# Performance work log

Hardware: AMD Instinct MI355X
Metric: run time of the kernel (lower is better)

## Reference

```python
import jax, jax.numpy as jnp
import numpy as np

B, T, J, E = 64, 512, 64, 128
D = 2 * E  # bidaf feature dim


def _lstm_dir(x, Wih, Whh, bih, bhh, reverse):
    # x: (B, S, I); PyTorch gate order i, f, g, o
    H = Whh.shape[1]
    b = bih + bhh
    xs = jnp.swapaxes(x, 0, 1)  # (S, B, I)
    if reverse:
        xs = xs[::-1]
    pre = jnp.einsum('sbi,gi->sbg', xs, Wih) + b  # precompute input projections
    h0 = jnp.zeros((x.shape[0], H), x.dtype)

    def step(carry, pt):
        h, c = carry
        gates = pt + h @ Whh.T
        i, f, g, o = jnp.split(gates, 4, axis=-1)
        c = jax.nn.sigmoid(f) * c + jax.nn.sigmoid(i) * jnp.tanh(g)
        h = jax.nn.sigmoid(o) * jnp.tanh(c)
        return (h, c), h

    _, hs = jax.lax.scan(step, (h0, h0), pre)
    if reverse:
        hs = hs[::-1]
    return jnp.swapaxes(hs, 0, 1)  # (B, S, H)


def _bilstm(x, pf, pb):
    hf = _lstm_dir(x, pf[0], pf[1], pf[2], pf[3], False)
    hb = _lstm_dir(x, pb[0], pb[1], pb[2], pb[3], True)
    return jnp.concatenate([hf, hb], axis=-1)


def setup_inputs() -> dict:
    key = jax.random.key(0)
    ks = iter(jax.random.split(key, 40))

    def rn(shape, scale=0.05):
        return jax.random.normal(next(ks), shape, jnp.float32) * scale

    inp = {
        'c': jax.random.normal(next(ks), (B, T, D), jnp.float32),
        'q': jax.random.normal(next(ks), (B, J, D), jnp.float32),
        # trilinear attention weights (Linear(2E,1) each)
        'wc': rn((D,)), 'bc': rn((1,)),
        'wq': rn((D,)), 'bq': rn((1,)),
        'wcq': rn((D,)), 'bcq': rn((1,)),
        # modeling BiLSTM: input 8E -> hidden E, bidirectional
        'l1f_Wih': rn((4 * E, 8 * E)), 'l1f_Whh': rn((4 * E, E)), 'l1f_bih': rn((4 * E,)), 'l1f_bhh': rn((4 * E,)),
        'l1b_Wih': rn((4 * E, 8 * E)), 'l1b_Whh': rn((4 * E, E)), 'l1b_bih': rn((4 * E,)), 'l1b_bhh': rn((4 * E,)),
        # output BiLSTM: input 2E -> hidden E, bidirectional
        'l2f_Wih': rn((4 * E, 2 * E)), 'l2f_Whh': rn((4 * E, E)), 'l2f_bih': rn((4 * E,)), 'l2f_bhh': rn((4 * E,)),
        'l2b_Wih': rn((4 * E, 2 * E)), 'l2b_Whh': rn((4 * E, E)), 'l2b_bih': rn((4 * E,)), 'l2b_bhh': rn((4 * E,)),
        # span predictors Linear(10E, 1)
        'W0': rn((10 * E,)), 'b0': rn((1,)),
        'W1': rn((10 * E,)), 'b1': rn((1,)),
    }
    return inp


def reference(c, q, wc, bc, wq, bq, wcq, bcq,
              l1f_Wih, l1f_Whh, l1f_bih, l1f_bhh,
              l1b_Wih, l1b_Whh, l1b_bih, l1b_bhh,
              l2f_Wih, l2f_Whh, l2f_bih, l2f_bhh,
              l2b_Wih, l2b_Whh, l2b_bih, l2b_bhh,
              W0, b0, W1, b1):
    # fused trilinear similarity: replaces the python loop over q_len
    cq = jnp.einsum('btd,bjd,d->btj', c, q, wcq) + bcq[0]            # (B,T,J)
    s = (c @ wc + bc[0])[:, :, None] + (q @ wq + bq[0])[:, None, :] + cq
    a = jax.nn.softmax(s, axis=2)
    c2q = jnp.einsum('btj,bjd->btd', a, q)                            # context-to-query
    b_att = jax.nn.softmax(jnp.max(s, axis=2), axis=1)                # (B,T)
    q2c = jnp.einsum('bt,btd->bd', b_att, c)[:, None, :]              # (B,1,2E) broadcast over T
    g = jnp.concatenate([c, c2q, c * c2q, c * q2c * jnp.ones_like(c)], axis=-1)  # (B,T,8E)

    m = _bilstm(g, (l1f_Wih, l1f_Whh, l1f_bih, l1f_bhh), (l1b_Wih, l1b_Whh, l1b_bih, l1b_bhh))
    p1 = jax.nn.softmax(jnp.concatenate([g, m], axis=-1) @ W0 + b0[0], axis=1)
    m2 = _bilstm(m, (l2f_Wih, l2f_Whh, l2f_bih, l2f_bhh), (l2b_Wih, l2b_Whh, l2b_bih, l2b_bhh))
    p2 = jax.nn.softmax(jnp.concatenate([g, m2], axis=-1) @ W1 + b1[0], axis=1)
    return (p1, p2)
```

## Files before the change

kernel.cpp:

```cpp
#include <hip/hip_runtime.h>
#include <hip/hip_bf16.h>
#include <cstdint>
#include <cstddef>


typedef short short8v __attribute__((ext_vector_type(8)));
typedef float f32x4 __attribute__((ext_vector_type(4)));
typedef unsigned short ushort8v __attribute__((ext_vector_type(8)));
typedef unsigned short ushort4v __attribute__((ext_vector_type(4)));

static __device__ __forceinline__ float bf2f(unsigned short u) {
  return __uint_as_float(((unsigned int)u) << 16);
}
static __device__ __forceinline__ unsigned short f2bf(float f) {
  unsigned int u = __float_as_uint(f);
  return (unsigned short)((u + 0x7FFFu + ((u >> 16) & 1u)) >> 16);
}
static __device__ __forceinline__ float fsig(float x) {
  return 1.f / (1.f + __expf(-x));
}
static __device__ __forceinline__ float ftanh(float x) {
  return 1.f - 2.f / (__expf(2.f * x) + 1.f);
}

__global__ __launch_bounds__(256) void cvt_w_kernel(
    const float* __restrict__ w1f, const float* __restrict__ w1b,
    const float* __restrict__ w2f, const float* __restrict__ w2b,
    const float* __restrict__ b1fi, const float* __restrict__ b1fh,
    const float* __restrict__ b1bi, const float* __restrict__ b1bh,
    const float* __restrict__ b2fi, const float* __restrict__ b2fh,
    const float* __restrict__ b2bi, const float* __restrict__ b2bh,
    unsigned short* __restrict__ d1f, unsigned short* __restrict__ d1b,
    unsigned short* __restrict__ d2f, unsigned short* __restrict__ d2b,
    float* __restrict__ bs)
{
  const int bid = blockIdx.x, tid = threadIdx.x;
  if (bid < 1280) {
    int idx = (bid * 256 + tid) * 4;
    const float* src;
    unsigned short* dst;
    int off;
    if (idx < 524288)        { src = w1f; dst = d1f; off = idx; }
    else if (idx < 1048576)  { src = w1b; dst = d1b; off = idx - 524288; }
    else if (idx < 1179648)  { src = w2f; dst = d2f; off = idx - 1048576; }
    else                     { src = w2b; dst = d2b; off = idx - 1179648; }
    float4 f = *(const float4*)(src + off);
    ushort4v v;
    v[0] = f2bf(f.x); v[1] = f2bf(f.y); v[2] = f2bf(f.z); v[3] = f2bf(f.w);
    *(ushort4v*)(dst + off) = v;
  } else {
    int bidx = (bid - 1280) * 256 + tid;
    int which = bidx >> 9, col = bidx & 511;
    float v;
    if (which == 0)      v = b1fi[col] + b1fh[col];
    else if (which == 1) v = b1bi[col] + b1bh[col];
    else if (which == 2) v = b2fi[col] + b2fh[col];
    else                 v = b2bi[col] + b2bh[col];
    bs[bidx] = v;
  }
}

__global__ __launch_bounds__(256) void attn_kernel(
    const float* __restrict__ c, const float* __restrict__ q,
    const float* __restrict__ wc, const float* __restrict__ bc,
    const float* __restrict__ wq, const float* __restrict__ bq,
    const float* __restrict__ wcq, const float* __restrict__ bcq,
    const float* __restrict__ W0, const float* __restrict__ W1,
    __hip_bfloat16* __restrict__ g, float* __restrict__ smax,
    float* __restrict__ gz0, float* __restrict__ gz1)
{
  __shared__ float qr[64][256];
  __shared__ float qrt[256][64];
  __shared__ float qwqs[64];
  __shared__ float cwbuf[4][256];
  __shared__ float abuf[4][64];
  const int b = blockIdx.x;
  const int tid = threadIdx.x;
  for (int e = tid; e < 64 * 256; e += 256) {
    int j = e >> 8, d = e & 255;
    float v = q[((size_t)b * 64 + j) * 256 + d];
    qr[j][d] = v;
    qrt[d][j] = v;
  }
  __syncthreads();
  if (tid < 64) {
    float s = 0.f;
    for (int d = 0; d < 256; ++d) s += qrt[d][tid] * wq[d];
    qwqs[tid] = s + bq[0];
  }
  __syncthreads();
  const int wave = tid >> 6, lane = tid & 63;
  const float bcv = bc[0], bcqv = bcq[0];
  const int t0 = blockIdx.y * 128;
  for (int it = 0; it < 32; ++it) {
    const int trow = t0 + wave + it * 4;
    const float* crow = c + ((size_t)b * 512 + trow) * 256;
    float cv[4];
    float part = 0.f;
    #pragma unroll
    for (int r = 0; r < 4; ++r) {
      int d = lane + 64 * r;
      cv[r] = crow[d];
      cwbuf[wave][d] = cv[r] * wcq[d];
      part += cv[r] * wc[d];
    }
    #pragma unroll
    for (int off = 32; off; off >>= 1) part += __shfl_xor(part, off);
    float s = part + bcv + qwqs[lane] + bcqv;
    #pragma unroll 8
    for (int d = 0; d < 256; ++d) s += cwbuf[wave][d] * qrt[d][lane];
    float mx = s;
    #pragma unroll
    for (int off = 32; off; off >>= 1) mx = fmaxf(mx, __shfl_xor(mx, off));
    float e = expf(s - mx);
    float sum = e;
    #pragma unroll
    for (int off = 32; off; off >>= 1) sum += __shfl_xor(sum, off);
    abuf[wave][lane] = e / sum;
    const size_t grow = (size_t)b * 512 + trow;
    if (lane == 0) smax[grow] = mx;
    size_t row = grow * 1024;
    float az0 = 0.f, az1 = 0.f;
    #pragma unroll
    for (int r = 0; r < 4; ++r) {
      int d = lane + 64 * r;
      float acc = 0.f;
      #pragma unroll 8
      for (int j = 0; j < 64; ++j) acc += abuf[wave][j] * qr[j][d];
      float prod = cv[r] * acc;
      g[row + d]       = __float2bfloat16(cv[r]);
      g[row + 256 + d] = __float2bfloat16(acc);
      g[row + 512 + d] = __float2bfloat16(prod);
      az0 += cv[r] * W0[d] + acc * W0[256 + d] + prod * W0[512 + d];
      az1 += cv[r] * W1[d] + acc * W1[256 + d] + prod * W1[512 + d];
    }
    #pragma unroll
    for (int off = 32; off; off >>= 1) {
      az0 += __shfl_xor(az0, off);
      az1 += __shfl_xor(az1, off);
    }
    if (lane == 0) { gz0[grow] = az0; gz1[grow] = az1; }
  }
}

__global__ __launch_bounds__(256) void batt_kernel(
    const float* __restrict__ c, const float* __restrict__ smax,
    const float* __restrict__ W0, const float* __restrict__ W1,
    __hip_bfloat16* __restrict__ g,
    float* __restrict__ gz0, float* __restrict__ gz1)
{
  __shared__ float sm[512];
  __shared__ float red[4], red2[4];
  __shared__ float q2c_s[256];
  const int b = blockIdx.x, tid = threadIdx.x;
  float v0 = smax[(size_t)b * 512 + tid];
  float v1 = smax[(size_t)b * 512 + tid + 256];
  float m = fmaxf(v0, v1);
  #pragma unroll
  for (int off = 32; off; off >>= 1) m = fmaxf(m, __shfl_xor(m, off));
  if ((tid & 63) == 0) red[tid >> 6] = m;
  __syncthreads();
  float M = fmaxf(fmaxf(red[0], red[1]), fmaxf(red[2], red[3]));
  float e0 = expf(v0 - M), e1 = expf(v1 - M);
  float ssum = e0 + e1;
  #pragma unroll
  for (int off = 32; off; off >>= 1) ssum += __shfl_xor(ssum, off);
  if ((tid & 63) == 0) red2[tid >> 6] = ssum;
  __syncthreads();
  float S = red2[0] + red2[1] + red2[2] + red2[3];
  sm[tid] = e0 / S;
  sm[tid + 256] = e1 / S;
  __syncthreads();
  float acc = 0.f;
  #pragma unroll 8
  for (int t = 0; t < 512; ++t) acc += sm[t] * c[((size_t)b * 512 + t) * 256 + tid];
  q2c_s[tid] = acc;
  __syncthreads();
  const int wave = tid >> 6, lane = tid & 63;
  float qv[4], w0c[4], w1c[4];
  #pragma unroll
  for (int r = 0; r < 4; ++r) {
    int d = lane + 64 * r;
    qv[r]  = q2c_s[d];
    w0c[r] = W0[768 + d];
    w1c[r] = W1[768 + d];
  }
  for (int t = wave; t < 512; t += 4) {
    size_t row = (size_t)b * 512 + t;
    float s0 = 0.f, s1 = 0.f;
    #pragma unroll
    for (int r = 0; r < 4; ++r) {
      int d = lane + 64 * r;
      float v = c[row * 256 + d];
      float gv = v * qv[r];
      g[row * 1024 + 768 + d] = __float2bfloat16(gv);
      s0 += gv * w0c[r];
      s1 += gv * w1c[r];
    }
    #pragma unroll
    for (int off = 32; off; off >>= 1) {
      s0 += __shfl_xor(s0, off);
      s1 += __shfl_xor(s1, off);
    }
    if (lane == 0) { gz0[row] += s0; gz1[row] += s1; }
  }
}

__global__ __launch_bounds__(256) void gemm_mfma_kernel(
    const __hip_bfloat16* __restrict__ Xg,
    const unsigned short* __restrict__ Wf, const unsigned short* __restrict__ Wb,
    const float* __restrict__ bsf, const float* __restrict__ bsb,
    __hip_bfloat16* __restrict__ Yf, __hip_bfloat16* __restrict__ Yb, int K)
{
  __shared__ unsigned short Xs[128 * 72];
  __shared__ unsigned short Ws[128 * 72];
  const unsigned short* X = (const unsigned short*)Xg;
  const unsigned short* W = blockIdx.z ? Wb : Wf;
  const float* bs = blockIdx.z ? bsb : bsf;
  __hip_bfloat16* Y = blockIdx.z ? Yb : Yf;
  const int tid = threadIdx.x;
  const int m0 = blockIdx.x * 128, n0 = blockIdx.y * 128;
  const int lane = tid & 63, wave = tid >> 6;
  const int wr = wave >> 1, wc = wave & 1;
  const int frow = lane & 15, fk = (lane >> 4) * 8;

  f32x4 acc[4][4] = {};
  for (int kt = 0; kt < K; kt += 64) {
    #pragma unroll
    for (int i = 0; i < 4; ++i) {
      int cidx = tid + 256 * i;
      int row = cidx >> 3, kc = cidx & 7;
      *(ushort8v*)&Xs[row * 72 + kc * 8] =
          *(const ushort8v*)&X[(size_t)(m0 + row) * K + kt + kc * 8];
      *(ushort8v*)&Ws[row * 72 + kc * 8] =
          *(const ushort8v*)&W[(size_t)(n0 + row) * K + kt + kc * 8];
    }
    __syncthreads();
    #pragma unroll
    for (int kk = 0; kk < 64; kk += 32) {
      short8v a[4], bfr[4];
      #pragma unroll
      for (int i = 0; i < 4; ++i)
        a[i] = *(const short8v*)&Xs[(wr * 64 + i * 16 + frow) * 72 + kk + fk];
      #pragma unroll
      for (int j = 0; j < 4; ++j)
        bfr[j] = *(const short8v*)&Ws[(wc * 64 + j * 16 + frow) * 72 + kk + fk];
      #pragma unroll
      for (int i = 0; i < 4; ++i)
        #pragma unroll
        for (int j = 0; j < 4; ++j)
          acc[i][j] = __builtin_amdgcn_mfma_f32_16x16x32_bf16(a[i], bfr[j], acc[i][j], 0, 0, 0);
    }
    __syncthreads();
  }
  const int r0 = (lane >> 4) * 4;
  #pragma unroll
  for (int j = 0; j < 4; ++j) {
    int col = n0 + wc * 64 + j * 16 + (lane & 15);
    int colp = (col & 127) * 4 + (col >> 7);
    float bsum = bs[col];
    #pragma unroll
    for (int i = 0; i < 4; ++i) {
      int rowb = m0 + wr * 64 + i * 16 + r0;
      #pragma unroll
      for (int r = 0; r < 4; ++r)
        Y[(size_t)(rowb + r) * 512 + colp] = __float2bfloat16(acc[i][j][r] + bsum);
    }
  }
}

__global__ __launch_bounds__(512, 2) void lstm_kernel(
    const __hip_bfloat16* __restrict__ pre_f, const __hip_bfloat16* __restrict__ pre_b,
    const float* __restrict__ Whh_f, const float* __restrict__ Whh_b,
    __hip_bfloat16* __restrict__ out)
{
  const int b = blockIdx.x, dir = blockIdx.y;
  const unsigned short* __restrict__ pre =
      (const unsigned short*)(dir ? pre_b : pre_f);
  const float* __restrict__ Whh = dir ? Whh_b : Whh_f;
  const int off = dir ? 128 : 0;
  const int tid = threadIdx.x;
  const int wave = tid >> 6, lane = tid & 63;
  const int cl = lane & 15;
  const int kg = lane >> 4;
  const int cell = wave * 16 + cl;

#define LOAD_BF(Q, T, DST)                                            \
  {                                                                   \
    const float* wp = Whh + (size_t)(Q * 128 + cell) * 128 + T * 32 + kg * 8; \
    float4 f0 = *(const float4*)wp;                                   \
    float4 f1 = *(const float4*)(wp + 4);                             \
    DST[0] = (short)f2bf(f0.x); DST[1] = (short)f2bf(f0.y);           \
    DST[2] = (short)f2bf(f0.z); DST[3] = (short)f2bf(f0.w);           \
    DST[4] = (short)f2bf(f1.x); DST[5] = (short)f2bf(f1.y);           \
    DST[6] = (short)f2bf(f1.z); DST[7] = (short)f2bf(f1.w);           \
    asm volatile("" : "+v"(DST));                                     \
  }
  short8v bf00, bf01, bf02, bf03, bf10, bf11, bf12, bf13;
  short8v bf20, bf21, bf22, bf23, bf30, bf31, bf32, bf33;
  LOAD_BF(0, 0, bf00) LOAD_BF(0, 1, bf01) LOAD_BF(0, 2, bf02) LOAD_BF(0, 3, bf03)
  LOAD_BF(1, 0, bf10) LOAD_BF(1, 1, bf11) LOAD_BF(1, 2, bf12) LOAD_BF(1, 3, bf13)
  LOAD_BF(2, 0, bf20) LOAD_BF(2, 1, bf21) LOAD_BF(2, 2, bf22) LOAD_BF(2, 3, bf23)
  LOAD_BF(3, 0, bf30) LOAD_BF(3, 1, bf31) LOAD_BF(3, 2, bf32) LOAD_BF(3, 3, bf33)
#undef LOAD_BF

  __shared__ unsigned short hbuf[2][128];
  if (tid < 128) { hbuf[0][tid] = 0; hbuf[1][tid] = 0; }
  __syncthreads();

  const size_t base = (size_t)b * 512;
  const int tstep = dir ? -1 : 1;
  const int t0 = dir ? 511 : 0;
  const unsigned short* prow = pre + base * 512 + cell * 4;
  unsigned short* orow = (unsigned short*)out + base * 256 + off + cell;

  int cur = 0;
  float cst = 0.f;
  f32x4 acc0 = {0.f, 0.f, 0.f, 0.f};
  f32x4 acc1 = acc0, acc2 = acc0, acc3 = acc0;

#define LSTM_STEP(P, HOUT)                                                  \
  {                                                                         \
    const unsigned short* hb = hbuf[cur];                                   \
    short8v a0 = *(const short8v*)(hb +  0 + kg * 8);                       \
    short8v a1 = *(const short8v*)(hb + 32 + kg * 8);                       \
    short8v a2 = *(const short8v*)(hb + 64 + kg * 8);                       \
    short8v a3 = *(const short8v*)(hb + 96 + kg * 8);                       \
    acc0[0] = bf2f(P[0]); acc1[0] = bf2f(P[1]);                             \
    acc2[0] = bf2f(P[2]); acc3[0] = bf2f(P[3]);                             \
    acc0 = __builtin_amdgcn_mfma_f32_16x16x32_bf16(a0, bf00, acc0, 0, 0, 0);\
    acc1 = __builtin_amdgcn_mfma_f32_16x16x32_bf16(a0, bf10, acc1, 0, 0, 0);\
    acc2 = __builtin_amdgcn_mfma_f32_16x16x32_bf16(a0, bf20, acc2, 0, 0, 0);\
    acc3 = __builtin_amdgcn_mfma_f32_16x16x32_bf16(a0, bf30, acc3, 0, 0, 0);\
    acc0 = __builtin_amdgcn_mfma_f32_16x16x32_bf16(a1, bf01, acc0, 0, 0, 0);\
    acc1 = __builtin_amdgcn_mfma_f32_16x16x32_bf16(a1, bf11, acc1, 0, 0, 0);\
    acc2 = __builtin_amdgcn_mfma_f32_16x16x32_bf16(a1, bf21, acc2, 0, 0, 0);\
    acc3 = __builtin_amdgcn_mfma_f32_16x16x32_bf16(a1, bf31, acc3, 0, 0, 0);\
    acc0 = __builtin_amdgcn_mfma_f32_16x16x32_bf16(a2, bf02, acc0, 0, 0, 0);\
    acc1 = __builtin_amdgcn_mfma_f32_16x16x32_bf16(a2, bf12, acc1, 0, 0, 0);\
    acc2 = __builtin_amdgcn_mfma_f32_16x16x32_bf16(a2, bf22, acc2, 0, 0, 0);\
    acc3 = __builtin_amdgcn_mfma_f32_16x16x32_bf16(a2, bf32, acc3, 0, 0, 0);\
    acc0 = __builtin_amdgcn_mfma_f32_16x16x32_bf16(a3, bf03, acc0, 0, 0, 0);\
    acc1 = __builtin_amdgcn_mfma_f32_16x16x32_bf16(a3, bf13, acc1, 0, 0, 0);\
    acc2 = __builtin_amdgcn_mfma_f32_16x16x32_bf16(a3, bf23, acc2, 0, 0, 0);\
    acc3 = __builtin_amdgcn_mfma_f32_16x16x32_bf16(a3, bf33, acc3, 0, 0, 0);\
    float gi_ = fsig(acc0[0]);                                              \
    float gf_ = fsig(acc1[0]);                                              \
    float gg_ = ftanh(acc2[0]);                                             \
    float go_ = fsig(acc3[0]);                                              \
    cst = gf_ * cst + gi_ * gg_;                                            \
    float hv = go_ * ftanh(cst);                                            \
    HOUT = f2bf(hv);                                                        \
    if (lane < 16) hbuf[cur ^ 1][cell] = HOUT;                              \
    __syncthreads();                                                        \
    cur ^= 1;                                                               \
  }

  for (int chunk = 0; chunk < 64; ++chunk) {
    const int tb = t0 + chunk * 8 * tstep;
    ushort4v p0 = *(const ushort4v*)(prow + (size_t)(tb)             * 512);
    ushort4v p1 = *(const ushort4v*)(prow + (size_t)(tb + 1 * tstep) * 512);
    ushort4v p2 = *(const ushort4v*)(prow + (size_t)(tb + 2 * tstep) * 512);
    ushort4v p3 = *(const ushort4v*)(prow + (size_t)(tb + 3 * tstep) * 512);
    ushort4v p4 = *(const ushort4v*)(prow + (size_t)(tb + 4 * tstep) * 512);
    ushort4v p5 = *(const ushort4v*)(prow + (size_t)(tb + 5 * tstep) * 512);
    ushort4v p6 = *(const ushort4v*)(prow + (size_t)(tb + 6 * tstep) * 512);
    ushort4v p7 = *(const ushort4v*)(prow + (size_t)(tb + 7 * tstep) * 512);
    unsigned short h0, h1, h2, h3, h4, h5, h6, h7;
    LSTM_STEP(p0, h0)
    LSTM_STEP(p1, h1)
    LSTM_STEP(p2, h2)
    LSTM_STEP(p3, h3)
    LSTM_STEP(p4, h4)
    LSTM_STEP(p5, h5)
    LSTM_STEP(p6, h6)
    LSTM_STEP(p7, h7)
    if (lane < 16) {
      orow[(size_t)(tb)             * 256] = h0;
      orow[(size_t)(tb + 1 * tstep) * 256] = h1;
      orow[(size_t)(tb + 2 * tstep) * 256] = h2;
      orow[(size_t)(tb + 3 * tstep) * 256] = h3;
      orow[(size_t)(tb + 4 * tstep) * 256] = h4;
      orow[(size_t)(tb + 5 * tstep) * 256] = h5;
      orow[(size_t)(tb + 6 * tstep) * 256] = h6;
      orow[(size_t)(tb + 7 * tstep) * 256] = h7;
    }
  }
#undef LSTM_STEP
}

__global__ __launch_bounds__(256) void logits_kernel(
    const __hip_bfloat16* __restrict__ m, const float* __restrict__ W,
    const float* __restrict__ bias, const float* __restrict__ gz,
    float* __restrict__ z)
{
  const int row = blockIdx.x * 4 + (threadIdx.x >> 6);
  const int lane = threadIdx.x & 63;
  const unsigned short* mrow = (const unsigned short*)m + (size_t)row * 256;
  float acc = 0.f;
  #pragma unroll
  for (int i = 0; i < 4; ++i) acc += bf2f(mrow[lane + 64 * i]) * W[1024 + lane + 64 * i];
  #pragma unroll
  for (int off = 32; off; off >>= 1) acc += __shfl_xor(acc, off);
  if (lane == 0) z[row] = acc + gz[row] + bias[0];
}

__global__ __launch_bounds__(512) void softmax_t_kernel(
    const float* __restrict__ z, float* __restrict__ p)
{
  const int b = blockIdx.x, t = threadIdx.x;
  __shared__ float red[8], red2[8];
  float v = z[(size_t)b * 512 + t];
  float m = v;
  #pragma unroll
  for (int off = 32; off; off >>= 1) m = fmaxf(m, __shfl_xor(m, off));
  if ((t & 63) == 0) red[t >> 6] = m;
  __syncthreads();
  float M = red[0];
  #pragma unroll
  for (int i = 1; i < 8; ++i) M = fmaxf(M, red[i]);
  float e = expf(v - M);
  float s = e;
  #pragma unroll
  for (int off = 32; off; off >>= 1) s += __shfl_xor(s, off);
  if ((t & 63) == 0) red2[t >> 6] = s;
  __syncthreads();
  float S = red2[0];
  #pragma unroll
  for (int i = 1; i < 8; ++i) S += red2[i];
  p[(size_t)b * 512 + t] = e / S;
}

extern "C" void kernel_launch(void* const* d_in, const int* in_sizes, int n_in,
                              void* d_out, int out_size, void* d_ws, size_t ws_size,
                              hipStream_t stream)
{
  const float* c   = (const float*)d_in[0];
  const float* q   = (const float*)d_in[1];
  const float* wc  = (const float*)d_in[2];
  const float* bc  = (const float*)d_in[3];
  const float* wq  = (const float*)d_in[4];
  const float* bq  = (const float*)d_in[5];
  const float* wcq = (const float*)d_in[6];
  const float* bcq = (const float*)d_in[7];
  const float* l1f_Wih = (const float*)d_in[8];
  const float* l1f_Whh = (const float*)d_in[9];
  const float* l1f_bih = (const float*)d_in[10];
  const float* l1f_bhh = (const float*)d_in[11];
  const float* l1b_Wih = (const float*)d_in[12];
  const float* l1b_Whh = (const float*)d_in[13];
  const float* l1b_bih = (const float*)d_in[14];
  const float* l1b_bhh = (const float*)d_in[15];
  const float* l2f_Wih = (const float*)d_in[16];
  const float* l2f_Whh = (const float*)d_in[17];
  const float* l2f_bih = (const float*)d_in[18];
  const float* l2f_bhh = (const float*)d_in[19];
  const float* l2b_Wih = (const float*)d_in[20];
  const float* l2b_Whh = (const float*)d_in[21];
  const float* l2b_bih = (const float*)d_in[22];
  const float* l2b_bhh = (const float*)d_in[23];
  const float* W0 = (const float*)d_in[24];
  const float* b0 = (const float*)d_in[25];
  const float* W1 = (const float*)d_in[26];
  const float* b1 = (const float*)d_in[27];

  const size_t required = 137371648u;
  if (ws_size < required) return;

  char* wsb = (char*)d_ws;
  __hip_bfloat16* gbf = (__hip_bfloat16*)wsb;
  __hip_bfloat16* m   = (__hip_bfloat16*)wsb;
  __hip_bfloat16* m2  = (__hip_bfloat16*)(wsb + 33554432);
  __hip_bfloat16* pref = (__hip_bfloat16*)(wsb + 67108864);
  __hip_bfloat16* preb = (__hip_bfloat16*)(wsb + 100663296);
  float* gz0  = (float*)(wsb + 134217728);
  float* gz1  = gz0 + 32768;
  float* smax = gz1 + 32768;
  float* z    = smax + 32768;
  unsigned short* w1f = (unsigned short*)(wsb + 134742016);
  unsigned short* w1b = (unsigned short*)(wsb + 135790592);
  unsigned short* w2f = (unsigned short*)(wsb + 136839168);
  unsigned short* w2b = (unsigned short*)(wsb + 137101312);
  float* bs = (float*)(wsb + 137363456);
  float* p1 = (float*)d_out;
  float* p2 = p1 + 32768;

  cvt_w_kernel<<<1288, 256, 0, stream>>>(l1f_Wih, l1b_Wih, l2f_Wih, l2b_Wih,
                                         l1f_bih, l1f_bhh, l1b_bih, l1b_bhh,
                                         l2f_bih, l2f_bhh, l2b_bih, l2b_bhh,
                                         w1f, w1b, w2f, w2b, bs);
  attn_kernel<<<dim3(64, 4), 256, 0, stream>>>(c, q, wc, bc, wq, bq, wcq, bcq,
                                               W0, W1, gbf, smax, gz0, gz1);
  batt_kernel<<<64, 256, 0, stream>>>(c, smax, W0, W1, gbf, gz0, gz1);

  gemm_mfma_kernel<<<dim3(256, 4, 2), 256, 0, stream>>>(
      gbf, w1f, w1b, bs, bs + 512, pref, preb, 1024);
  lstm_kernel<<<dim3(64, 2), 512, 0, stream>>>(pref, preb, l1f_Whh, l1b_Whh, m);

  logits_kernel<<<8192, 256, 0, stream>>>(m, W0, b0, gz0, z);
  softmax_t_kernel<<<64, 512, 0, stream>>>(z, p1);

  gemm_mfma_kernel<<<dim3(256, 4, 2), 256, 0, stream>>>(
      m, w2f, w2b, bs + 1024, bs + 1536, pref, preb, 256);
  lstm_kernel<<<dim3(64, 2), 512, 0, stream>>>(pref, preb, l2f_Whh, l2b_Whh, m2);

  logits_kernel<<<8192, 256, 0, stream>>>(m2, W1, b1, gz1, z);
  softmax_t_kernel<<<64, 512, 0, stream>>>(z, p2);
}
```

Before: 1.175 ms.

## Rewrite attention similarity and context-to-query products as bf16 MFMA tiles

The attention kernel now stages the context tile and query in LDS as bf16 and computes both the trilinear similarity and the softmax-weighted query sum with 16x16x32 bf16 MFMA instructions, processing 16-row tiles per wave. The c·wc term is folded into the query-side operand, and the row max and softmax are done with lane shuffles across MFMA output fragments. This replaces the scalar fp32 LDS dot-product loops. In exchange it adds bf16 rounding to the similarity scores and to the probabilities used for c2q, which may move the outputs away from the fp32 reference.

```diff
diff --git a/kernel.cpp b/kernel.cpp
--- a/kernel.cpp
+++ b/kernel.cpp
@@ -69,77 +69,153 @@
     __hip_bfloat16* __restrict__ g, float* __restrict__ smax,
     float* __restrict__ gz0, float* __restrict__ gz1)
 {
-  __shared__ float qr[64][256];
-  __shared__ float qrt[256][64];
+  __shared__ unsigned short cbf[128][264];
+  __shared__ unsigned short qhb[64][264];
+  __shared__ unsigned short qtb[256][72];
+  __shared__ unsigned short Pbuf[4][16][72];
   __shared__ float qwqs[64];
-  __shared__ float cwbuf[4][256];
-  __shared__ float abuf[4][64];
-  const int b = blockIdx.x;
-  const int tid = threadIdx.x;
-  for (int e = tid; e < 64 * 256; e += 256) {
-    int j = e >> 8, d = e & 255;
-    float v = q[((size_t)b * 64 + j) * 256 + d];
-    qr[j][d] = v;
-    qrt[d][j] = v;
-  }
-  __syncthreads();
-  if (tid < 64) {
+  __shared__ float qwp[4][64];
+  const int b = blockIdx.x, tid = threadIdx.x;
+  const int wave = tid >> 6, lane = tid & 63;
+  const int t0 = blockIdx.y * 128;
+  unsigned short* gbase = (unsigned short*)g;
+
+  #pragma unroll
+  for (int i = 0; i < 16; ++i) {
+    int idx = tid + i * 256;
+    int j = idx >> 6, d4 = (idx & 63) * 4;
+    float4 v = *(const float4*)&q[((size_t)b * 64 + j) * 256 + d4];
+    float4 w4 = *(const float4*)&wcq[d4];
+    float4 c4 = *(const float4*)&wc[d4];
+    qhb[j][d4 + 0] = f2bf(v.x * w4.x + c4.x);
+    qhb[j][d4 + 1] = f2bf(v.y * w4.y + c4.y);
+    qhb[j][d4 + 2] = f2bf(v.z * w4.z + c4.z);
+    qhb[j][d4 + 3] = f2bf(v.w * w4.w + c4.w);
+    qtb[d4 + 0][j] = f2bf(v.x);
+    qtb[d4 + 1][j] = f2bf(v.y);
+    qtb[d4 + 2][j] = f2bf(v.z);
+    qtb[d4 + 3][j] = f2bf(v.w);
+  }
+  #pragma unroll
+  for (int i = 0; i < 32; ++i) {
+    int idx = tid + i * 256;
+    int r = idx >> 6, d4 = (idx & 63) * 4;
+    float4 v = *(const float4*)&c[((size_t)b * 512 + t0 + r) * 256 + d4];
+    ushort4v u;
+    u[0] = f2bf(v.x); u[1] = f2bf(v.y); u[2] = f2bf(v.z); u[3] = f2bf(v.w);
+    *(ushort4v*)&cbf[r][d4] = u;
+    *(ushort4v*)&gbase[((size_t)b * 512 + t0 + r) * 1024 + d4] = u;
+  }
+  __syncthreads();
+  {
     float s = 0.f;
-    for (int d = 0; d < 256; ++d) s += qrt[d][tid] * wq[d];
-    qwqs[tid] = s + bq[0];
-  }
-  __syncthreads();
-  const int wave = tid >> 6, lane = tid & 63;
-  const float bcv = bc[0], bcqv = bcq[0];
-  const int t0 = blockIdx.y * 128;
-  for (int it = 0; it < 32; ++it) {
-    const int trow = t0 + wave + it * 4;
-    const float* crow = c + ((size_t)b * 512 + trow) * 256;
-    float cv[4];
-    float part = 0.f;
-    #pragma unroll
-    for (int r = 0; r < 4; ++r) {
-      int d = lane + 64 * r;
-      cv[r] = crow[d];
-      cwbuf[wave][d] = cv[r] * wcq[d];
-      part += cv[r] * wc[d];
-    }
-    #pragma unroll
-    for (int off = 32; off; off >>= 1) part += __shfl_xor(part, off);
-    float s = part + bcv + qwqs[lane] + bcqv;
-    #pragma unroll 8
-    for (int d = 0; d < 256; ++d) s += cwbuf[wave][d] * qrt[d][lane];
-    float mx = s;
-    #pragma unroll
-    for (int off = 32; off; off >>= 1) mx = fmaxf(mx, __shfl_xor(mx, off));
-    float e = expf(s - mx);
-    float sum = e;
-    #pragma unroll
-    for (int off = 32; off; off >>= 1) sum += __shfl_xor(sum, off);
-    abuf[wave][lane] = e / sum;
-    const size_t grow = (size_t)b * 512 + trow;
-    if (lane == 0) smax[grow] = mx;
-    size_t row = grow * 1024;
-    float az0 = 0.f, az1 = 0.f;
-    #pragma unroll
-    for (int r = 0; r < 4; ++r) {
-      int d = lane + 64 * r;
-      float acc = 0.f;
-      #pragma unroll 8
-      for (int j = 0; j < 64; ++j) acc += abuf[wave][j] * qr[j][d];
-      float prod = cv[r] * acc;
-      g[row + d]       = __float2bfloat16(cv[r]);
-      g[row + 256 + d] = __float2bfloat16(acc);
-      g[row + 512 + d] = __float2bfloat16(prod);
-      az0 += cv[r] * W0[d] + acc * W0[256 + d] + prod * W0[512 + d];
-      az1 += cv[r] * W1[d] + acc * W1[256 + d] + prod * W1[512 + d];
-    }
-    #pragma unroll
-    for (int off = 32; off; off >>= 1) {
-      az0 += __shfl_xor(az0, off);
-      az1 += __shfl_xor(az1, off);
-    }
-    if (lane == 0) { gz0[grow] = az0; gz1[grow] = az1; }
+    for (int dd = 0; dd < 64; ++dd) {
+      int d = wave * 64 + dd;
+      s += bf2f(qtb[d][lane]) * wq[d];
+    }
+    qwp[wave][lane] = s;
+  }
+  __syncthreads();
+  if (tid < 64) qwqs[tid] = qwp[0][tid] + qwp[1][tid] + qwp[2][tid] + qwp[3][tid] + bq[0];
+  __syncthreads();
+
+  const int cl = lane & 15, kg = lane >> 4;
+  const float sbias = bc[0] + bcq[0];
+
+  #pragma unroll
+  for (int half = 0; half < 2; ++half) {
+    const int tt = wave + half * 4;
+    const int rowb = tt * 16;
+    f32x4 acc[4] = {};
+    #pragma unroll
+    for (int kt = 0; kt < 8; ++kt) {
+      short8v a = *(const short8v*)&cbf[rowb + cl][kt * 32 + kg * 8];
+      #pragma unroll
+      for (int jt = 0; jt < 4; ++jt) {
+        short8v bq_ = *(const short8v*)&qhb[jt * 16 + cl][kt * 32 + kg * 8];
+        acc[jt] = __builtin_amdgcn_mfma_f32_16x16x32_bf16(a, bq_, acc[jt], 0, 0, 0);
+      }
+    }
+    #pragma unroll
+    for (int jt = 0; jt < 4; ++jt) {
+      float qadd = qwqs[jt * 16 + cl] + sbias;
+      #pragma unroll
+      for (int r = 0; r < 4; ++r) acc[jt][r] += qadd;
+    }
+    f32x4 mx = acc[0];
+    #pragma unroll
+    for (int jt = 1; jt < 4; ++jt)
+      #pragma unroll
+      for (int r = 0; r < 4; ++r) mx[r] = fmaxf(mx[r], acc[jt][r]);
+    #pragma unroll
+    for (int off = 1; off < 16; off <<= 1)
+      #pragma unroll
+      for (int r = 0; r < 4; ++r) mx[r] = fmaxf(mx[r], __shfl_xor(mx[r], off));
+    f32x4 se = {0.f, 0.f, 0.f, 0.f};
+    #pragma unroll
+    for (int jt = 0; jt < 4; ++jt)
+      #pragma unroll
+      for (int r = 0; r < 4; ++r) {
+        acc[jt][r] = __expf(acc[jt][r] - mx[r]);
+        se[r] += acc[jt][r];
+      }
+    #pragma unroll
+    for (int off = 1; off < 16; off <<= 1)
+      #pragma unroll
+      for (int r = 0; r < 4; ++r) se[r] += __shfl_xor(se[r], off);
+    f32x4 inv;
+    #pragma unroll
+    for (int r = 0; r < 4; ++r) inv[r] = 1.f / se[r];
+    #pragma unroll
+    for (int jt = 0; jt < 4; ++jt)
+      #pragma unroll
+      for (int r = 0; r < 4; ++r)
+        Pbuf[wave][4 * kg + r][jt * 16 + cl] = f2bf(acc[jt][r] * inv[r]);
+    if (cl == 0) {
+      #pragma unroll
+      for (int r = 0; r < 4; ++r)
+        smax[(size_t)b * 512 + t0 + rowb + 4 * kg + r] = mx[r];
+    }
+    f32x4 gz0p = {0.f, 0.f, 0.f, 0.f}, gz1p = {0.f, 0.f, 0.f, 0.f};
+    for (int dt = 0; dt < 16; ++dt) {
+      f32x4 ca = {0.f, 0.f, 0.f, 0.f};
+      #pragma unroll
+      for (int kt = 0; kt < 2; ++kt) {
+        short8v pa = *(const short8v*)&Pbuf[wave][cl][kt * 32 + kg * 8];
+        short8v qb_ = *(const short8v*)&qtb[dt * 16 + cl][kt * 32 + kg * 8];
+        ca = __builtin_amdgcn_mfma_f32_16x16x32_bf16(pa, qb_, ca, 0, 0, 0);
+      }
+      int d = dt * 16 + cl;
+      float w0a = W0[d], w0b_ = W0[256 + d], w0c2 = W0[512 + d];
+      float w1a = W1[d], w1b2 = W1[256 + d], w1c2 = W1[512 + d];
+      #pragma unroll
+      for (int r = 0; r < 4; ++r) {
+        int rloc = rowb + 4 * kg + r;
+        float cv = bf2f(cbf[rloc][d]);
+        float av = ca[r];
+        float pr = cv * av;
+        size_t gr = ((size_t)b * 512 + t0 + rloc) * 1024;
+        gbase[gr + 256 + d] = f2bf(av);
+        gbase[gr + 512 + d] = f2bf(pr);
+        gz0p[r] += cv * w0a + av * w0b_ + pr * w0c2;
+        gz1p[r] += cv * w1a + av * w1b2 + pr * w1c2;
+      }
+    }
+    #pragma unroll
+    for (int off = 1; off < 16; off <<= 1)
+      #pragma unroll
+      for (int r = 0; r < 4; ++r) {
+        gz0p[r] += __shfl_xor(gz0p[r], off);
+        gz1p[r] += __shfl_xor(gz1p[r], off);
+      }
+    if (cl == 0) {
+      #pragma unroll
+      for (int r = 0; r < 4; ++r) {
+        size_t rw = (size_t)b * 512 + t0 + rowb + 4 * kg + r;
+        gz0[rw] = gz0p[r];
+        gz1[rw] = gz1p[r];
+      }
+    }
   }
 }
 
```

After: 967.1 us. 1.21x faster.
